# Performance work log

Hardware: AMD Instinct MI355X
Metric: run time of the kernel (lower is better)

The kernel has to match this reference:

```python
import jax, jax.numpy as jnp
import numpy as np

K_UPPER = 196608  # number of smallest-|grad| positions to mask per sample


def setup_inputs() -> dict:
    key = jax.random.key(0)
    k1, k2 = jax.random.split(key)
    x = jax.random.normal(k1, (64, 3, 512, 512), dtype=jnp.float32)
    grad = jax.random.normal(k2, (64, 3, 512, 512), dtype=jnp.float32)
    return {"x": x, "grad": grad}


def _mask_low_gradient(x, grad):
    # x, grad: [B, C, H, W]
    B, C, H, W = x.shape
    hw = H * W
    flat_g = grad.reshape(B, -1)                                  # [B, C*H*W]
    # _sort: k smallest absolute gradients -> top_k of negated abs (unsorted ok)
    _neg_vals, idx = jax.lax.top_k(-jnp.abs(flat_g), K_UPPER)     # idx: [B, K]
    # channel containing each selected flat index (matches the torch range test)
    ch = idx // hw                                                # [B, K]
    xc = x.reshape(B, C, hw)
    # Faithful to source: torch slice [start:channel_indexes] EXCLUDES the last
    # element of each channel when computing min/max.
    mn = jnp.min(xc[:, :, : hw - 1], axis=-1)                     # [B, C]
    mx = jnp.max(xc[:, :, : hw - 1], axis=-1)                     # [B, C]
    lo = jnp.take_along_axis(mn, ch, axis=1)                      # [B, K]
    hi = jnp.take_along_axis(mx, ch, axis=1)                      # [B, K]
    # uniform fill in [lo, hi) per masked element
    u = jax.random.uniform(jax.random.key(42), idx.shape, dtype=x.dtype)
    fill = lo + u * (hi - lo)                                     # [B, K]
    flat_x = x.reshape(B, -1)
    out = flat_x.at[jnp.arange(B)[:, None], idx].set(fill)
    return out.reshape(x.shape)


def reference(x, grad):
    return _mask_low_gradient(x, grad)
```

## Files before the change

kernel.cpp:

```cpp
#include <hip/hip_runtime.h>
#include <stdint.h>

#define TPB 256
#define TPS 1024

constexpr int BN   = 64;
constexpr int CCH  = 3;
constexpr int HWS  = 262144;
constexpr int LOG_HW = 18;
constexpr int NPS  = 786432;
constexpr int KSEL = 196608;
constexpr int KCAP = 200704;
constexpr int NB_T = 32;
constexpr int CH_T = NPS / NB_T;
constexpr int NB_C = 64;
constexpr int CH_C = NPS / NB_C;
constexpr int WCH  = CH_C / 4;
constexpr int NB_S = 8;
constexpr int CH_S = KCAP / NB_S;
constexpr int TILE = 4096;
constexpr int NBINS = 2048;
constexpr int SUB  = 8;

typedef unsigned u32x4 __attribute__((ext_vector_type(4)));

constexpr int WS_MN   = 0;
constexpr int WS_MX   = 192;
constexpr int WS_V1   = 384;
constexpr int WS_B1   = 448;
constexpr int WS_GS   = 512;
constexpr int WS_KP   = 576;
constexpr int WS_S0   = 640;
constexpr int WS_S01  = 704;
constexpr int WS_CNT  = 768;
constexpr int WS_COFF = WS_CNT + BN * 256;
constexpr int WS_MNP  = WS_COFF + BN * 256;
constexpr int WS_MXP  = WS_MNP + BN * CCH * SUB;
constexpr int WS_CHC  = WS_MXP + BN * CCH * SUB;
constexpr int WS_THA  = WS_CHC + BN * 4;
constexpr int WS_THB  = WS_THA + BN * NBINS;
constexpr int WS_H0   = WS_THB + BN * NBINS;
constexpr int WS_H1   = WS_H0 + BN * 256 * NB_S;
constexpr int WS_H2   = WS_H1 + BN * 256 * NB_S;
constexpr int WS_H3   = WS_H2 + BN * 256 * NB_S;
constexpr size_t WS_FIX_END = (size_t)WS_H3 + (size_t)BN * 256 * NB_S;
constexpr size_t RECW = (size_t)BN * KCAP * 2;
constexpr size_t WS_NEEDED_BYTES = (WS_FIX_END + 2 * RECW) * 4;

__device__ __forceinline__ unsigned rotl32(unsigned x, int r) { return (x << r) | (x >> (32 - r)); }

__device__ __forceinline__ void tf4(unsigned& x0, unsigned& x1, int a, int b, int c, int d) {
  x0 += x1; x1 = rotl32(x1, a); x1 ^= x0;
  x0 += x1; x1 = rotl32(x1, b); x1 ^= x0;
  x0 += x1; x1 = rotl32(x1, c); x1 ^= x0;
  x0 += x1; x1 = rotl32(x1, d); x1 ^= x0;
}

__device__ __forceinline__ void threefry2x32(unsigned k0, unsigned k1, unsigned c0, unsigned c1,
                                             unsigned& o0, unsigned& o1) {
  const unsigned ks2 = k0 ^ k1 ^ 0x1BD11BDAu;
  unsigned x0 = c0 + k0, x1 = c1 + k1;
  tf4(x0, x1, 13, 15, 26, 6);  x0 += k1;  x1 += ks2 + 1u;
  tf4(x0, x1, 17, 29, 16, 24); x0 += ks2; x1 += k0 + 2u;
  tf4(x0, x1, 13, 15, 26, 6);  x0 += k0;  x1 += k1 + 3u;
  tf4(x0, x1, 17, 29, 16, 24); x0 += k1;  x1 += ks2 + 4u;
  tf4(x0, x1, 13, 15, 26, 6);  x0 += ks2; x1 += k0 + 5u;
  o0 = x0; o1 = x1;
}

__global__ __launch_bounds__(TPB) void k_zero(unsigned* __restrict__ p, int n) {
  int i = blockIdx.x * TPB + threadIdx.x;
  if (i < n) p[i] = 0u;
}

__global__ __launch_bounds__(TPB) void k_mnmx(const float4* __restrict__ x,
                                              unsigned* __restrict__ ws) {
  __shared__ float smn[TPB], smx[TPB];
  const int g = blockIdx.x;
  const int bc = g / SUB, sub = g - bc * SUB;
  const int Q4 = HWS / 4 / SUB;
  const size_t base4 = (size_t)bc * (HWS / 4) + (size_t)sub * Q4;
  const bool last = (sub == SUB - 1);
  const int tid = threadIdx.x;
  float lo = 3.4e38f, hi = -3.4e38f;
  for (int i = tid; i < Q4; i += TPB) {
    float4 v = x[base4 + i];
    if (last && i == Q4 - 1) {
      lo = fminf(lo, fminf(fminf(v.x, v.y), v.z));
      hi = fmaxf(hi, fmaxf(fmaxf(v.x, v.y), v.z));
    } else {
      lo = fminf(lo, fminf(fminf(v.x, v.y), fminf(v.z, v.w)));
      hi = fmaxf(hi, fmaxf(fmaxf(v.x, v.y), fmaxf(v.z, v.w)));
    }
  }
  smn[tid] = lo; smx[tid] = hi; __syncthreads();
  for (int s = TPB / 2; s > 0; s >>= 1) {
    if (tid < s) { smn[tid] = fminf(smn[tid], smn[tid + s]); smx[tid] = fmaxf(smx[tid], smx[tid + s]); }
    __syncthreads();
  }
  if (tid == 0) {
    ((float*)(ws + WS_MNP))[g] = smn[0];
    ((float*)(ws + WS_MXP))[g] = smx[0];
  }
}

__global__ __launch_bounds__(TPB) void k_mnfin(unsigned* __restrict__ ws) {
  const int t = threadIdx.x;
  if (t < BN * CCH) {
    const float* mnp = (const float*)(ws + WS_MNP);
    const float* mxp = (const float*)(ws + WS_MXP);
    float lo = 3.4e38f, hi = -3.4e38f;
    for (int s = 0; s < SUB; ++s) {
      lo = fminf(lo, mnp[t * SUB + s]);
      hi = fmaxf(hi, mxp[t * SUB + s]);
    }
    ((float*)(ws + WS_MN))[t] = lo;
    ((float*)(ws + WS_MX))[t] = hi;
  }
}

__global__ __launch_bounds__(TPB) void k_thrA(const unsigned* __restrict__ gb, unsigned* __restrict__ hist) {
  __shared__ unsigned h[NBINS];
  const int b = blockIdx.y, blk = blockIdx.x, tid = threadIdx.x;
  for (int v = tid; v < NBINS; v += TPB) h[v] = 0u;
  __syncthreads();
  const uint4* g4 = (const uint4*)(gb + (size_t)b * NPS + (size_t)blk * CH_T);
  for (int i = tid; i < CH_T / 4; i += TPB) {
    uint4 v = g4[i];
    atomicAdd(&h[(v.x & 0x7FFFFFFFu) >> 21], 1u);
    atomicAdd(&h[(v.y & 0x7FFFFFFFu) >> 21], 1u);
    atomicAdd(&h[(v.z & 0x7FFFFFFFu) >> 21], 1u);
    atomicAdd(&h[(v.w & 0x7FFFFFFFu) >> 21], 1u);
  }
  __syncthreads();
  unsigned* gh = hist + (size_t)b * NBINS;
  for (int v = tid; v < NBINS; v += TPB) if (h[v]) atomicAdd(&gh[v], h[v]);
}

__global__ __launch_bounds__(TPB) void k_thrB(const unsigned* __restrict__ gb,
                                              unsigned* __restrict__ hist,
                                              const unsigned* __restrict__ ws) {
  __shared__ unsigned h[NBINS];
  const int b = blockIdx.y, blk = blockIdx.x, tid = threadIdx.x;
  for (int v = tid; v < NBINS; v += TPB) h[v] = 0u;
  __syncthreads();
  const unsigned sel = ws[WS_V1 + b];
  const uint4* g4 = (const uint4*)(gb + (size_t)b * NPS + (size_t)blk * CH_T);
  for (int i = tid; i < CH_T / 4; i += TPB) {
    uint4 v = g4[i];
    unsigned a0 = v.x & 0x7FFFFFFFu, a1 = v.y & 0x7FFFFFFFu;
    unsigned a2 = v.z & 0x7FFFFFFFu, a3 = v.w & 0x7FFFFFFFu;
    if ((a0 >> 21) == sel) atomicAdd(&h[(a0 >> 10) & 2047u], 1u);
    if ((a1 >> 21) == sel) atomicAdd(&h[(a1 >> 10) & 2047u], 1u);
    if ((a2 >> 21) == sel) atomicAdd(&h[(a2 >> 10) & 2047u], 1u);
    if ((a3 >> 21) == sel) atomicAdd(&h[(a3 >> 10) & 2047u], 1u);
  }
  __syncthreads();
  unsigned* gh = hist + (size_t)b * NBINS;
  for (int v = tid; v < NBINS; v += TPB) if (h[v]) atomicAdd(&gh[v], h[v]);
}

__global__ __launch_bounds__(TPB) void k_find(const unsigned* __restrict__ hist,
                                              unsigned* __restrict__ ws, int mode) {
  __shared__ unsigned part[TPB];
  const int b = blockIdx.x, tid = threadIdx.x;
  const unsigned* h = hist + (size_t)b * NBINS;
  const int per = NBINS / TPB;
  const unsigned Kt = (mode == 0) ? (unsigned)KSEL : (unsigned)KSEL - ws[WS_B1 + b];
  unsigned vals[8];
  unsigned s = 0;
  for (int j = 0; j < per; ++j) { vals[j] = h[tid * per + j]; s += vals[j]; }
  part[tid] = s; __syncthreads();
  for (int off = 1; off < TPB; off <<= 1) {
    unsigned t = (tid >= off) ? part[tid - off] : 0u;
    __syncthreads(); part[tid] += t; __syncthreads();
  }
  unsigned run = part[tid] - s;
  for (int j = 0; j < per; ++j) {
    const unsigned lo = run, c = vals[j];
    run += c;
    if (lo < Kt && Kt <= run) {
      const unsigned v = (unsigned)(tid * per + j);
      if (mode == 0) {
        ws[WS_V1 + b] = v; ws[WS_B1 + b] = lo;
      } else {
        const unsigned T22 = (ws[WS_V1 + b] << 11) | v;
        ws[WS_GS + b] = (T22 << 10) | 1023u;
        unsigned kp = ws[WS_B1 + b] + lo + c;
        if (kp > (unsigned)KCAP) kp = (unsigned)KCAP;
        ws[WS_KP + b] = kp;
      }
    }
  }
}

__global__ __launch_bounds__(TPB) void k_ccount(const unsigned* __restrict__ gb, unsigned* __restrict__ ws) {
  __shared__ unsigned chs[3];
  const int bid = blockIdx.x;
  const int b = bid & 63, blk = bid >> 6, tid = threadIdx.x;
  const int lane = tid & 63, wv = tid >> 6;
  if (tid < 3) chs[tid] = 0u;
  __syncthreads();
  const unsigned G = ws[WS_GS + b];
  const uint4* g4 = (const uint4*)(gb + (size_t)b * NPS + (size_t)blk * CH_C) + wv * (WCH / 4);
  const unsigned e0 = (unsigned)blk * CH_C + (unsigned)wv * WCH;
  unsigned cnt = 0, cc0 = 0, cc1 = 0, cc2 = 0;
  for (int it = 0; it < WCH / 256; ++it) {
    const uint4 v = g4[it * 64 + lane];
    const unsigned e = e0 + (unsigned)it * 256u + (unsigned)lane * 4u;
    const unsigned k[4] = { v.x & 0x7FFFFFFFu, v.y & 0x7FFFFFFFu, v.z & 0x7FFFFFFFu, v.w & 0x7FFFFFFFu };
#pragma unroll
    for (int c = 0; c < 4; ++c) {
      if (k[c] <= G) {
        ++cnt;
        const unsigned ch = (e + (unsigned)c) >> LOG_HW;
        if (ch == 0) ++cc0; else if (ch == 1) ++cc1; else ++cc2;
      }
    }
  }
  for (int off = 32; off >= 1; off >>= 1) cnt += __shfl_down(cnt, off, 64);
  if (lane == 0) ws[WS_CNT + b * 256 + blk * 4 + wv] = cnt;
  if (cc0) atomicAdd(&chs[0], cc0);
  if (cc1) atomicAdd(&chs[1], cc1);
  if (cc2) atomicAdd(&chs[2], cc2);
  __syncthreads();
  if (tid < 3 && chs[tid]) atomicAdd(&ws[WS_CHC + b * 4 + tid], chs[tid]);
}

__global__ __launch_bounds__(TPB) void k_cscan(unsigned* __restrict__ ws) {
  __shared__ unsigned wsum[4];
  const int b = blockIdx.x, tid = threadIdx.x;
  const int lane = tid & 63, wv = tid >> 6;
  const unsigned cnt = ws[WS_CNT + b * 256 + tid];
  unsigned incl = cnt;
  for (int off = 1; off < 64; off <<= 1) {
    unsigned t = __shfl_up(incl, off, 64);
    if (lane >= off) incl += t;
  }
  if (lane == 63) wsum[wv] = incl;
  __syncthreads();
  unsigned wpre = 0;
  for (int w = 0; w < wv; ++w) wpre += wsum[w];
  ws[WS_COFF + b * 256 + tid] = incl - cnt + wpre;
  if (tid == 0) {
    const unsigned s0 = ws[WS_CHC + b * 4 + 0];
    ws[WS_S0 + b] = s0;
    ws[WS_S01 + b] = s0 + ws[WS_CHC + b * 4 + 1];
  }
}

__global__ __launch_bounds__(TPB) void k_cscatter(const unsigned* __restrict__ gb,
                                                  const unsigned* __restrict__ ws,
                                                  unsigned* __restrict__ keyArr,
                                                  unsigned* __restrict__ H0) {
  __shared__ unsigned h2[256 * NB_S];
  const int bid = blockIdx.x;
  const int b = bid & 63, blk = bid >> 6, tid = threadIdx.x;
  const int lane = tid & 63, wv = tid >> 6;
  for (int e = tid; e < 256 * NB_S; e += TPB) h2[e] = 0u;
  __syncthreads();
  const unsigned G = ws[WS_GS + b];
  unsigned base = ws[WS_COFF + b * 256 + blk * 4 + wv];
  const uint4* g4 = (const uint4*)(gb + (size_t)b * NPS + (size_t)blk * CH_C) + wv * (WCH / 4);
  unsigned* ka = keyArr + (size_t)b * KCAP;
  for (int it = 0; it < WCH / 256; ++it) {
    const uint4 v = g4[it * 64 + lane];
    unsigned k[4] = { v.x & 0x7FFFFFFFu, v.y & 0x7FFFFFFFu, v.z & 0x7FFFFFFFu, v.w & 0x7FFFFFFFu };
    bool s[4];
    unsigned cnt = 0;
#pragma unroll
    for (int c = 0; c < 4; ++c) { s[c] = (k[c] <= G); cnt += (unsigned)s[c]; }
    unsigned incl = cnt;
    for (int off = 1; off < 64; off <<= 1) {
      unsigned u = __shfl_up(incl, off, 64);
      if (lane >= off) incl += u;
    }
    const unsigned wtot = __shfl(incl, 63, 64);
    unsigned pos = base + incl - cnt;
#pragma unroll
    for (int c = 0; c < 4; ++c) {
      if (s[c]) {
        if (pos < (unsigned)KCAP) {
          ka[pos] = k[c];
          atomicAdd(&h2[(k[c] & 255u) * NB_S + pos / (unsigned)CH_S], 1u);
        }
        ++pos;
      }
    }
    base += wtot;
  }
  __syncthreads();
  unsigned* Hb = H0 + (size_t)b * 256 * NB_S;
  for (int e = tid; e < 256 * NB_S; e += TPB) {
    unsigned c = h2[e];
    if (c) atomicAdd(&Hb[e], c);
  }
}

__global__ __launch_bounds__(TPB) void k_hscan(unsigned* __restrict__ H) {
  __shared__ unsigned wsum[4];
  const int b = blockIdx.x, tid = threadIdx.x;
  const int lane = tid & 63, wv = tid >> 6;
  unsigned* Hb = H + (size_t)b * 256 * NB_S;
  unsigned row[NB_S];
  unsigned run = 0;
#pragma unroll
  for (int k = 0; k < NB_S; ++k) {
    unsigned t = Hb[tid * NB_S + k];
    row[k] = run; run += t;
  }
  unsigned incl = run;
  for (int off = 1; off < 64; off <<= 1) {
    unsigned t = __shfl_up(incl, off, 64);
    if (lane >= off) incl += t;
  }
  if (lane == 63) wsum[wv] = incl;
  __syncthreads();
  unsigned wpre = 0;
  for (int w = 0; w < wv; ++w) wpre += wsum[w];
  const unsigned excl = incl - run + wpre;
#pragma unroll
  for (int k = 0; k < NB_S; ++k) Hb[tid * NB_S + k] = row[k] + excl;
}

template<int MODE>
__global__ __launch_bounds__(TPS) void k_sort8(const unsigned* __restrict__ keyIn,
                                               const uint2* __restrict__ inR,
                                               uint2* __restrict__ outR,
                                               unsigned* __restrict__ fillmap,
                                               const unsigned* __restrict__ Hcur,
                                               unsigned* __restrict__ Hnext,
                                               const unsigned* __restrict__ ws,
                                               int shift) {
  constexpr int DBITS = (MODE == 2) ? 7 : 8;
  constexpr unsigned DMASK = (1u << DBITS) - 1u;
  __shared__ unsigned wh[16][256];
  __shared__ unsigned gout[256];
  __shared__ unsigned gbase[256];
  __shared__ unsigned wsum[4];
  __shared__ uint2    stg[(MODE == 2) ? 1 : TILE];
  __shared__ unsigned h2[(MODE == 2) ? 1 : 256 * NB_S];
  const int bid = blockIdx.x;
  const int b = bid & 63, blk = bid >> 6, tid = threadIdx.x;
  const int lane = tid & 63, wv = tid >> 6;
  const unsigned long long ltm = (1ull << lane) - 1ull;
  const unsigned kp = min(ws[WS_KP + b], (unsigned)KCAP);
  const unsigned s0 = (unsigned)blk * CH_S;
  const unsigned s1 = min(s0 + (unsigned)CH_S, kp);
  const unsigned* ki = keyIn + (size_t)b * KCAP;
  const uint2* in = inR + (size_t)b * KCAP;
  uint2* out = outR + (size_t)b * KCAP;
  unsigned* fm = fillmap + (size_t)b * KCAP;

  unsigned S0 = 0, S01 = 0;
  float l0 = 0, l1 = 0, l2 = 0, h0 = 0, h1 = 0, h2v = 0;
  if (MODE == 2) {
    S0 = ws[WS_S0 + b]; S01 = ws[WS_S01 + b];
    const float* mnf = (const float*)(ws + WS_MN);
    const float* mxf = (const float*)(ws + WS_MX);
    l0 = mnf[b * CCH]; l1 = mnf[b * CCH + 1]; l2 = mnf[b * CCH + 2];
    h0 = mxf[b * CCH]; h1 = mxf[b * CCH + 1]; h2v = mxf[b * CCH + 2];
  }

  for (int d = tid; d < 256; d += TPS) gbase[d] = Hcur[((size_t)b * 256 + d) * NB_S + blk];
  if (MODE != 2) for (int e = tid; e < 256 * NB_S; e += TPS) h2[e] = 0u;
  __syncthreads();

  for (unsigned t0 = s0; t0 < s1; t0 += (unsigned)TILE) {
    { uint4* w4 = (uint4*)&wh[0][0];
      w4[tid] = make_uint4(0u, 0u, 0u, 0u); }
    __syncthreads();

    unsigned key[4], cpp[4], wloc[4], dig[4];
    bool val[4];
    const unsigned wbase = t0 + (unsigned)wv * 256u;
#pragma unroll
    for (int c = 0; c < 4; ++c) {
      const unsigned i = wbase + (unsigned)c * 64u + (unsigned)lane;
      val[c] = (i < s1);
      if (MODE == 0) { cpp[c] = i; key[c] = val[c] ? ki[i] : 0u; }
      else { uint2 r = val[c] ? in[i] : make_uint2(0u, 0u); cpp[c] = r.x; key[c] = r.y; }
      dig[c] = (key[c] >> shift) & DMASK;
      unsigned long long peers = __ballot(val[c]);
#pragma unroll
      for (int bit = 0; bit < DBITS; ++bit) {
        unsigned long long bb = __ballot(val[c] && ((dig[c] >> bit) & 1u));
        peers &= ((dig[c] >> bit) & 1u) ? bb : ~bb;
      }
      const unsigned before = (unsigned)__popcll(peers & ltm);
      int ldr = __ffsll((unsigned long long)peers) - 1;
      if (ldr < 0) ldr = 0;
      unsigned old = 0;
      if (val[c] && lane == ldr) old = atomicAdd(&wh[wv][dig[c]], (unsigned)__popcll(peers));
      old = __shfl(old, ldr, 64);
      wloc[c] = old + before;
    }
    __syncthreads();

    unsigned incl = 0, tot = 0;
    if (tid < 256) {
      const unsigned d = (unsigned)tid;
#pragma unroll
      for (int w = 0; w < 16; ++w) tot += wh[w][d];
      incl = tot;
      for (int off = 1; off < 64; off <<= 1) {
        unsigned t = __shfl_up(incl, off, 64);
        if (lane >= off) incl += t;
      }
      if (lane == 63) wsum[wv] = incl;
    }
    __syncthreads();
    if (tid < 256) {
      const unsigned d = (unsigned)tid;
      unsigned wpre = 0;
      for (int w = 0; w < wv; ++w) wpre += wsum[w];
      const unsigned tstart = incl - tot + wpre;
      const unsigned g = gbase[d];
      gout[d] = g - tstart;
      gbase[d] = g + tot;
      unsigned run = tstart;
#pragma unroll
      for (int w = 0; w < 16; ++w) { const unsigned t = wh[w][d]; wh[w][d] = run; run += t; }
    }
    __syncthreads();

    if (MODE != 2) {
#pragma unroll
      for (int c = 0; c < 4; ++c) {
        if (val[c]) {
          uint2 r; r.x = cpp[c]; r.y = key[c];
          stg[wh[wv][dig[c]] + wloc[c]] = r;
        }
      }
      __syncthreads();
      const unsigned nt = min((unsigned)TILE, s1 - t0);
      for (unsigned j = tid; j < nt; j += TPS) {
        const uint2 r = stg[j];
        const unsigned d = (r.y >> shift) & 255u;
        const unsigned pos = gout[d] + j;
        out[pos] = r;
        const unsigned nd = (r.y >> (shift + 8)) & 255u;
        atomicAdd(&h2[nd * NB_S + pos / (unsigned)CH_S], 1u);
      }
    } else {
#pragma unroll
      for (int c = 0; c < 4; ++c) {
        if (val[c]) {
          const unsigned rank = gout[dig[c]] + wh[wv][dig[c]] + wloc[c];
          unsigned res = 0xFFFFFFFFu;
          if (rank < (unsigned)KSEL) {
            const unsigned p = (unsigned)b * (unsigned)KSEL + rank;
            unsigned o0, o1;
            threefry2x32(0u, 42u, 0u, p, o0, o1);
            const unsigned bits = o0 ^ o1;
            const float u = __uint_as_float((bits >> 9) | 0x3f800000u) - 1.0f;
            const unsigned ch = (unsigned)(cpp[c] >= S0) + (unsigned)(cpp[c] >= S01);
            const float lo = (ch == 0) ? l0 : ((ch == 1) ? l1 : l2);
            const float hi = (ch == 0) ? h0 : ((ch == 1) ? h1 : h2v);
            res = __float_as_uint(lo + u * (hi - lo));
          }
          fm[cpp[c]] = res;
        }
      }
    }
    __syncthreads();
  }

  if (MODE != 2) {
    unsigned* Hb = Hnext + (size_t)b * 256 * NB_S;
    for (int e = tid; e < 256 * NB_S; e += TPS) {
      unsigned c = h2[e];
      if (c) atomicAdd(&Hb[e], c);
    }
  }
}

__global__ __launch_bounds__(TPB) void k_fill(const u32x4* __restrict__ x4,
                                              const u32x4* __restrict__ g4all,
                                              const unsigned* __restrict__ fillmap,
                                              const unsigned* __restrict__ ws,
                                              u32x4* __restrict__ out4) {
  const int bid = blockIdx.x;
  const int b = bid & 63, blk = bid >> 6, tid = threadIdx.x;
  const int lane = tid & 63, wv = tid >> 6;
  const unsigned G = ws[WS_GS + b];
  const unsigned kp = min(ws[WS_KP + b], (unsigned)KCAP);
  unsigned base = ws[WS_COFF + b * 256 + blk * 4 + wv];
  const size_t t4 = (size_t)b * (NPS / 4) + (size_t)blk * (CH_C / 4) + (size_t)wv * (WCH / 4);
  const unsigned* fm = fillmap + (size_t)b * KCAP;
  for (int it = 0; it < WCH / 256; ++it) {
    const size_t a = t4 + it * 64 + lane;
    const u32x4 gv = __builtin_nontemporal_load(&g4all[a]);
    u32x4 xv = __builtin_nontemporal_load(&x4[a]);
    unsigned k[4] = { gv.x & 0x7FFFFFFFu, gv.y & 0x7FFFFFFFu, gv.z & 0x7FFFFFFFu, gv.w & 0x7FFFFFFFu };
    bool s[4];
    unsigned cnt = 0;
#pragma unroll
    for (int c = 0; c < 4; ++c) { s[c] = (k[c] <= G); cnt += (unsigned)s[c]; }
    unsigned incl = cnt;
    for (int off = 1; off < 64; off <<= 1) {
      unsigned u = __shfl_up(incl, off, 64);
      if (lane >= off) incl += u;
    }
    const unsigned wtot = __shfl(incl, 63, 64);
    unsigned pos = base + incl - cnt;
#pragma unroll
    for (int c = 0; c < 4; ++c) {
      if (s[c]) {
        if (pos < kp) {
          const unsigned r = fm[pos];
          if (r != 0xFFFFFFFFu) xv[c] = r;
        }
        ++pos;
      }
    }
    __builtin_nontemporal_store(xv, &out4[a]);
    base += wtot;
  }
}

extern "C" void kernel_launch(void* const* d_in, const int* in_sizes, int n_in,
                              void* d_out, int out_size, void* d_ws, size_t ws_size,
                              hipStream_t stream) {
  const float* x = (const float*)d_in[0];
  const unsigned* gb = (const unsigned*)d_in[1];
  float* out = (float*)d_out;
  unsigned* ws = (unsigned*)d_ws;
  if (ws_size < WS_NEEDED_BYTES) return;

  unsigned* R1 = ws + WS_FIX_END;
  unsigned* R2 = ws + WS_FIX_END + RECW;
  unsigned* H0 = ws + WS_H0;
  unsigned* H1 = ws + WS_H1;
  unsigned* H2 = ws + WS_H2;
  unsigned* H3 = ws + WS_H3;

  dim3 blk(TPB);
  dim3 sblk(TPS);

  k_mnmx<<<dim3(BN * CCH * SUB), blk, 0, stream>>>((const float4*)x, ws);
  k_mnfin<<<dim3(1), blk, 0, stream>>>(ws);
  {
    const int nz = (int)(WS_FIX_END - WS_CHC);
    k_zero<<<dim3((nz + TPB - 1) / TPB), blk, 0, stream>>>(ws + WS_CHC, nz);
  }

  k_thrA<<<dim3(NB_T, BN), blk, 0, stream>>>(gb, ws + WS_THA);
  k_find<<<dim3(BN), blk, 0, stream>>>(ws + WS_THA, ws, 0);
  k_thrB<<<dim3(NB_T, BN), blk, 0, stream>>>(gb, ws + WS_THB, ws);
  k_find<<<dim3(BN), blk, 0, stream>>>(ws + WS_THB, ws, 1);

  k_ccount<<<dim3(NB_C * BN), blk, 0, stream>>>(gb, ws);
  k_cscan<<<dim3(BN), blk, 0, stream>>>(ws);
  k_cscatter<<<dim3(NB_C * BN), blk, 0, stream>>>(gb, ws, R1, H0);

  k_hscan<<<dim3(BN), blk, 0, stream>>>(H0);
  k_sort8<0><<<dim3(NB_S * BN), sblk, 0, stream>>>(R1, (const uint2*)nullptr, (uint2*)R2, nullptr, H0, H1, ws, 0);
  k_hscan<<<dim3(BN), blk, 0, stream>>>(H1);
  k_sort8<1><<<dim3(NB_S * BN), sblk, 0, stream>>>(nullptr, (const uint2*)R2, (uint2*)R1, nullptr, H1, H2, ws, 8);
  k_hscan<<<dim3(BN), blk, 0, stream>>>(H2);
  k_sort8<1><<<dim3(NB_S * BN), sblk, 0, stream>>>(nullptr, (const uint2*)R1, (uint2*)R2, nullptr, H2, H3, ws, 16);
  k_hscan<<<dim3(BN), blk, 0, stream>>>(H3);
  k_sort8<2><<<dim3(NB_S * BN), sblk, 0, stream>>>(nullptr, (const uint2*)R2, (uint2*)nullptr, R1, H3, nullptr, ws, 24);

  k_fill<<<dim3(NB_C * BN), blk, 0, stream>>>((const u32x4*)x, (const u32x4*)gb, R1, ws, (u32x4*)out);
}
```

Measured before the change: 768.6 us.

## Replace scattered fillmap writes with bucketed pair scatter and local unpack

The final radix pass used to write fill values straight into the fillmap at random candidate positions. It now runs a dedicated k_final kernel that computes the rank-based fill values and then buckets (position, value) pairs by position block of 4096, using histograms gathered during the third sort pass. A new k_unpack kernel then scatters each bucket through shared memory and writes the fillmap with coalesced stores. The aim is to turn uncoalesced global scatter writes into coalesced ones, at the cost of an extra kernel, an extra scan, extra histogram atomics and a round trip through the pair buffer.

New measurement: 774.0 us. Within noise of the previous version (+0.7%).

```diff
diff --git a/kernel.cpp b/kernel.cpp
--- a/kernel.cpp
+++ b/kernel.cpp
@@ -21,6 +21,7 @@
 constexpr int TILE = 4096;
 constexpr int NBINS = 2048;
 constexpr int SUB  = 8;
+constexpr int NFB  = 49;
 
 typedef unsigned u32x4 __attribute__((ext_vector_type(4)));
 
@@ -43,7 +44,8 @@
 constexpr int WS_H1   = WS_H0 + BN * 256 * NB_S;
 constexpr int WS_H2   = WS_H1 + BN * 256 * NB_S;
 constexpr int WS_H3   = WS_H2 + BN * 256 * NB_S;
-constexpr size_t WS_FIX_END = (size_t)WS_H3 + (size_t)BN * 256 * NB_S;
+constexpr int WS_HF   = WS_H3 + BN * 256 * NB_S;
+constexpr size_t WS_FIX_END = (size_t)WS_HF + (size_t)BN * 64 * NB_S;
 constexpr size_t RECW = (size_t)BN * KCAP * 2;
 constexpr size_t WS_NEEDED_BYTES = (WS_FIX_END + 2 * RECW) * 4;
 
@@ -323,23 +325,46 @@
   for (int k = 0; k < NB_S; ++k) Hb[tid * NB_S + k] = row[k] + excl;
 }
 
+__global__ __launch_bounds__(64) void k_hscanF(unsigned* __restrict__ Hf) {
+  const int b = blockIdx.x, tid = threadIdx.x;
+  unsigned* Hb = Hf + (size_t)b * 64 * NB_S;
+  unsigned row[NB_S];
+  unsigned run = 0;
+  if (tid < NFB) {
+#pragma unroll
+    for (int k = 0; k < NB_S; ++k) {
+      unsigned t = Hb[tid * NB_S + k];
+      row[k] = run; run += t;
+    }
+  }
+  unsigned incl = run;
+  for (int off = 1; off < 64; off <<= 1) {
+    unsigned t = __shfl_up(incl, off, 64);
+    if (tid >= off) incl += t;
+  }
+  const unsigned excl = incl - run;
+  if (tid < NFB) {
+#pragma unroll
+    for (int k = 0; k < NB_S; ++k) Hb[tid * NB_S + k] = row[k] + excl;
+  }
+}
+
 template<int MODE>
 __global__ __launch_bounds__(TPS) void k_sort8(const unsigned* __restrict__ keyIn,
                                                const uint2* __restrict__ inR,
                                                uint2* __restrict__ outR,
-                                               unsigned* __restrict__ fillmap,
                                                const unsigned* __restrict__ Hcur,
                                                unsigned* __restrict__ Hnext,
+                                               unsigned* __restrict__ Hf,
                                                const unsigned* __restrict__ ws,
                                                int shift) {
-  constexpr int DBITS = (MODE == 2) ? 7 : 8;
-  constexpr unsigned DMASK = (1u << DBITS) - 1u;
   __shared__ unsigned wh[16][256];
   __shared__ unsigned gout[256];
   __shared__ unsigned gbase[256];
   __shared__ unsigned wsum[4];
-  __shared__ uint2    stg[(MODE == 2) ? 1 : TILE];
-  __shared__ unsigned h2[(MODE == 2) ? 1 : 256 * NB_S];
+  __shared__ uint2    stg[TILE];
+  __shared__ unsigned h2[256 * NB_S];
+  __shared__ unsigned h2f[(MODE == 1) ? NFB * NB_S : 1];
   const int bid = blockIdx.x;
   const int b = bid & 63, blk = bid >> 6, tid = threadIdx.x;
   const int lane = tid & 63, wv = tid >> 6;
@@ -350,20 +375,11 @@
   const unsigned* ki = keyIn + (size_t)b * KCAP;
   const uint2* in = inR + (size_t)b * KCAP;
   uint2* out = outR + (size_t)b * KCAP;
-  unsigned* fm = fillmap + (size_t)b * KCAP;
-
-  unsigned S0 = 0, S01 = 0;
-  float l0 = 0, l1 = 0, l2 = 0, h0 = 0, h1 = 0, h2v = 0;
-  if (MODE == 2) {
-    S0 = ws[WS_S0 + b]; S01 = ws[WS_S01 + b];
-    const float* mnf = (const float*)(ws + WS_MN);
-    const float* mxf = (const float*)(ws + WS_MX);
-    l0 = mnf[b * CCH]; l1 = mnf[b * CCH + 1]; l2 = mnf[b * CCH + 2];
-    h0 = mxf[b * CCH]; h1 = mxf[b * CCH + 1]; h2v = mxf[b * CCH + 2];
-  }
+  const bool doF = (MODE == 1) && (Hf != nullptr);
 
   for (int d = tid; d < 256; d += TPS) gbase[d] = Hcur[((size_t)b * 256 + d) * NB_S + blk];
-  if (MODE != 2) for (int e = tid; e < 256 * NB_S; e += TPS) h2[e] = 0u;
+  for (int e = tid; e < 256 * NB_S; e += TPS) h2[e] = 0u;
+  if (MODE == 1) { if (doF) for (int e = tid; e < NFB * NB_S; e += TPS) h2f[e] = 0u; }
   __syncthreads();
 
   for (unsigned t0 = s0; t0 < s1; t0 += (unsigned)TILE) {
@@ -380,10 +396,10 @@
       val[c] = (i < s1);
       if (MODE == 0) { cpp[c] = i; key[c] = val[c] ? ki[i] : 0u; }
       else { uint2 r = val[c] ? in[i] : make_uint2(0u, 0u); cpp[c] = r.x; key[c] = r.y; }
-      dig[c] = (key[c] >> shift) & DMASK;
+      dig[c] = (key[c] >> shift) & 255u;
       unsigned long long peers = __ballot(val[c]);
 #pragma unroll
-      for (int bit = 0; bit < DBITS; ++bit) {
+      for (int bit = 0; bit < 8; ++bit) {
         unsigned long long bb = __ballot(val[c] && ((dig[c] >> bit) & 1u));
         peers &= ((dig[c] >> bit) & 1u) ? bb : ~bb;
       }
@@ -424,55 +440,210 @@
     }
     __syncthreads();
 
-    if (MODE != 2) {
-#pragma unroll
-      for (int c = 0; c < 4; ++c) {
-        if (val[c]) {
-          uint2 r; r.x = cpp[c]; r.y = key[c];
-          stg[wh[wv][dig[c]] + wloc[c]] = r;
-        }
-      }
-      __syncthreads();
-      const unsigned nt = min((unsigned)TILE, s1 - t0);
-      for (unsigned j = tid; j < nt; j += TPS) {
-        const uint2 r = stg[j];
-        const unsigned d = (r.y >> shift) & 255u;
-        const unsigned pos = gout[d] + j;
-        out[pos] = r;
-        const unsigned nd = (r.y >> (shift + 8)) & 255u;
-        atomicAdd(&h2[nd * NB_S + pos / (unsigned)CH_S], 1u);
-      }
-    } else {
-#pragma unroll
-      for (int c = 0; c < 4; ++c) {
-        if (val[c]) {
-          const unsigned rank = gout[dig[c]] + wh[wv][dig[c]] + wloc[c];
-          unsigned res = 0xFFFFFFFFu;
-          if (rank < (unsigned)KSEL) {
-            const unsigned p = (unsigned)b * (unsigned)KSEL + rank;
-            unsigned o0, o1;
-            threefry2x32(0u, 42u, 0u, p, o0, o1);
-            const unsigned bits = o0 ^ o1;
-            const float u = __uint_as_float((bits >> 9) | 0x3f800000u) - 1.0f;
-            const unsigned ch = (unsigned)(cpp[c] >= S0) + (unsigned)(cpp[c] >= S01);
-            const float lo = (ch == 0) ? l0 : ((ch == 1) ? l1 : l2);
-            const float hi = (ch == 0) ? h0 : ((ch == 1) ? h1 : h2v);
-            res = __float_as_uint(lo + u * (hi - lo));
-          }
-          fm[cpp[c]] = res;
-        }
-      }
-    }
-    __syncthreads();
-  }
-
-  if (MODE != 2) {
+#pragma unroll
+    for (int c = 0; c < 4; ++c) {
+      if (val[c]) {
+        uint2 r; r.x = cpp[c]; r.y = key[c];
+        stg[wh[wv][dig[c]] + wloc[c]] = r;
+      }
+    }
+    __syncthreads();
+    const unsigned nt = min((unsigned)TILE, s1 - t0);
+    for (unsigned j = tid; j < nt; j += TPS) {
+      const uint2 r = stg[j];
+      const unsigned d = (r.y >> shift) & 255u;
+      const unsigned pos = gout[d] + j;
+      out[pos] = r;
+      const unsigned nd = (r.y >> (shift + 8)) & 255u;
+      atomicAdd(&h2[nd * NB_S + pos / (unsigned)CH_S], 1u);
+      if (doF) atomicAdd(&h2f[(r.x >> 12) * NB_S + pos / (unsigned)CH_S], 1u);
+    }
+    __syncthreads();
+  }
+
+  {
     unsigned* Hb = Hnext + (size_t)b * 256 * NB_S;
     for (int e = tid; e < 256 * NB_S; e += TPS) {
       unsigned c = h2[e];
       if (c) atomicAdd(&Hb[e], c);
     }
-  }
+    if (doF) {
+      unsigned* Hfb = Hf + (size_t)b * 64 * NB_S;
+      for (int e = tid; e < NFB * NB_S; e += TPS) {
+        unsigned c = h2f[e];
+        if (c) atomicAdd(&Hfb[e], c);
+      }
+    }
+  }
+}
+
+__global__ __launch_bounds__(TPS) void k_final(const uint2* __restrict__ inR,
+                                               uint2* __restrict__ pairOut,
+                                               const unsigned* __restrict__ Hcur,
+                                               const unsigned* __restrict__ Hf,
+                                               const unsigned* __restrict__ ws) {
+  __shared__ unsigned wh[16][128];
+  __shared__ unsigned gbase[128];
+  __shared__ unsigned whF[16][64];
+  __shared__ unsigned goutF[64];
+  __shared__ unsigned gbaseF[64];
+  __shared__ uint2    stg[TILE];
+  const int bid = blockIdx.x;
+  const int b = bid & 63, blk = bid >> 6, tid = threadIdx.x;
+  const int lane = tid & 63, wv = tid >> 6;
+  const unsigned long long ltm = (1ull << lane) - 1ull;
+  const unsigned kp = min(ws[WS_KP + b], (unsigned)KCAP);
+  const unsigned s0 = (unsigned)blk * CH_S;
+  const unsigned s1 = min(s0 + (unsigned)CH_S, kp);
+  const uint2* in = inR + (size_t)b * KCAP;
+  uint2* po = pairOut + (size_t)b * KCAP;
+
+  const unsigned S0 = ws[WS_S0 + b], S01 = ws[WS_S01 + b];
+  const float* mnf = (const float*)(ws + WS_MN);
+  const float* mxf = (const float*)(ws + WS_MX);
+  const float l0 = mnf[b * CCH], l1 = mnf[b * CCH + 1], l2 = mnf[b * CCH + 2];
+  const float h0 = mxf[b * CCH], h1 = mxf[b * CCH + 1], h2v = mxf[b * CCH + 2];
+
+  for (int d = tid; d < 128; d += TPS) gbase[d] = Hcur[((size_t)b * 256 + d) * NB_S + blk];
+  for (int d = tid; d < 64; d += TPS)
+    gbaseF[d] = (d < NFB) ? Hf[((size_t)b * 64 + d) * NB_S + blk] : 0u;
+  __syncthreads();
+
+  for (unsigned t0 = s0; t0 < s1; t0 += (unsigned)TILE) {
+    { uint4* p = (uint4*)&wh[0][0];
+      if (tid < 512) p[tid] = make_uint4(0u, 0u, 0u, 0u);
+      uint4* q = (uint4*)&whF[0][0];
+      if (tid >= 512 && tid < 768) q[tid - 512] = make_uint4(0u, 0u, 0u, 0u); }
+    __syncthreads();
+
+    unsigned key[4], cpp[4], wloc[4], dig[4];
+    bool val[4];
+    const unsigned wbase = t0 + (unsigned)wv * 256u;
+#pragma unroll
+    for (int c = 0; c < 4; ++c) {
+      const unsigned i = wbase + (unsigned)c * 64u + (unsigned)lane;
+      val[c] = (i < s1);
+      uint2 r = val[c] ? in[i] : make_uint2(0u, 0u);
+      cpp[c] = r.x; key[c] = r.y;
+      dig[c] = (key[c] >> 24) & 127u;
+      unsigned long long peers = __ballot(val[c]);
+#pragma unroll
+      for (int bit = 0; bit < 7; ++bit) {
+        unsigned long long bb = __ballot(val[c] && ((dig[c] >> bit) & 1u));
+        peers &= ((dig[c] >> bit) & 1u) ? bb : ~bb;
+      }
+      const unsigned before = (unsigned)__popcll(peers & ltm);
+      int ldr = __ffsll((unsigned long long)peers) - 1;
+      if (ldr < 0) ldr = 0;
+      unsigned old = 0;
+      if (val[c] && lane == ldr) old = atomicAdd(&wh[wv][dig[c]], (unsigned)__popcll(peers));
+      old = __shfl(old, ldr, 64);
+      wloc[c] = old + before;
+    }
+    __syncthreads();
+
+    if (tid < 128) {
+      const unsigned d = (unsigned)tid;
+      unsigned run = gbase[d];
+#pragma unroll
+      for (int w = 0; w < 16; ++w) { const unsigned t = wh[w][d]; wh[w][d] = run; run += t; }
+      gbase[d] = run;
+    }
+    __syncthreads();
+
+    unsigned vfill[4], dbF[4], wlocF[4];
+#pragma unroll
+    for (int c = 0; c < 4; ++c) {
+      if (val[c]) {
+        const unsigned rank = wh[wv][dig[c]] + wloc[c];
+        unsigned res = 0xFFFFFFFFu;
+        if (rank < (unsigned)KSEL) {
+          const unsigned p = (unsigned)b * (unsigned)KSEL + rank;
+          unsigned o0, o1;
+          threefry2x32(0u, 42u, 0u, p, o0, o1);
+          const unsigned bits = o0 ^ o1;
+          const float u = __uint_as_float((bits >> 9) | 0x3f800000u) - 1.0f;
+          const unsigned ch = (unsigned)(cpp[c] >= S0) + (unsigned)(cpp[c] >= S01);
+          const float lo = (ch == 0) ? l0 : ((ch == 1) ? l1 : l2);
+          const float hi = (ch == 0) ? h0 : ((ch == 1) ? h1 : h2v);
+          res = __float_as_uint(lo + u * (hi - lo));
+        }
+        vfill[c] = res;
+      }
+      dbF[c] = cpp[c] >> 12;
+      unsigned long long peers = __ballot(val[c]);
+#pragma unroll
+      for (int bit = 0; bit < 6; ++bit) {
+        unsigned long long bb = __ballot(val[c] && ((dbF[c] >> bit) & 1u));
+        peers &= ((dbF[c] >> bit) & 1u) ? bb : ~bb;
+      }
+      const unsigned before = (unsigned)__popcll(peers & ltm);
+      int ldr = __ffsll((unsigned long long)peers) - 1;
+      if (ldr < 0) ldr = 0;
+      unsigned old = 0;
+      if (val[c] && lane == ldr) old = atomicAdd(&whF[wv][dbF[c]], (unsigned)__popcll(peers));
+      old = __shfl(old, ldr, 64);
+      wlocF[c] = old + before;
+    }
+    __syncthreads();
+
+    if (tid < 64) {
+      const unsigned d = (unsigned)tid;
+      unsigned tot = 0;
+      if (d < NFB) {
+#pragma unroll
+        for (int w = 0; w < 16; ++w) tot += whF[w][d];
+      }
+      unsigned incl = tot;
+      for (int off = 1; off < 64; off <<= 1) {
+        unsigned t = __shfl_up(incl, off, 64);
+        if (lane >= off) incl += t;
+      }
+      const unsigned tstart = incl - tot;
+      goutF[d] = gbaseF[d] - tstart;
+      gbaseF[d] += tot;
+      unsigned run = tstart;
+#pragma unroll
+      for (int w = 0; w < 16; ++w) { const unsigned t = whF[w][d]; whF[w][d] = run; run += t; }
+    }
+    __syncthreads();
+
+#pragma unroll
+    for (int c = 0; c < 4; ++c) {
+      if (val[c]) {
+        uint2 r; r.x = cpp[c]; r.y = vfill[c];
+        stg[whF[wv][dbF[c]] + wlocF[c]] = r;
+      }
+    }
+    __syncthreads();
+
+    const unsigned nt = min((unsigned)TILE, s1 - t0);
+    for (unsigned j = tid; j < nt; j += TPS) {
+      const uint2 r = stg[j];
+      po[goutF[r.x >> 12] + j] = r;
+    }
+    __syncthreads();
+  }
+}
+
+__global__ __launch_bounds__(TPB) void k_unpack(const uint2* __restrict__ pairs,
+                                                unsigned* __restrict__ fm,
+                                                const unsigned* __restrict__ ws) {
+  __shared__ unsigned vals[4096];
+  const int bid = blockIdx.x;
+  const int b = bid & 63, d = bid >> 6, tid = threadIdx.x;
+  const unsigned kp = min(ws[WS_KP + b], (unsigned)KCAP);
+  const unsigned start = (unsigned)d * 4096u;
+  if (start >= kp) return;
+  const unsigned cnt = min(4096u, kp - start);
+  const uint2* pb = pairs + (size_t)b * KCAP + start;
+  for (unsigned j = tid; j < cnt; j += TPB) {
+    const uint2 r = pb[j];
+    vals[r.x & 4095u] = r.y;
+  }
+  __syncthreads();
+  unsigned* f = fm + (size_t)b * KCAP + start;
+  for (unsigned j = tid; j < cnt; j += TPB) f[j] = vals[j];
 }
 
 __global__ __launch_bounds__(TPB) void k_fill(const u32x4* __restrict__ x4,
@@ -534,6 +705,7 @@
   unsigned* H1 = ws + WS_H1;
   unsigned* H2 = ws + WS_H2;
   unsigned* H3 = ws + WS_H3;
+  unsigned* HF = ws + WS_HF;
 
   dim3 blk(TPB);
   dim3 sblk(TPS);
@@ -555,13 +727,16 @@
   k_cscatter<<<dim3(NB_C * BN), blk, 0, stream>>>(gb, ws, R1, H0);
 
   k_hscan<<<dim3(BN), blk, 0, stream>>>(H0);
-  k_sort8<0><<<dim3(NB_S * BN), sblk, 0, stream>>>(R1, (const uint2*)nullptr, (uint2*)R2, nullptr, H0, H1, ws, 0);
+  k_sort8<0><<<dim3(NB_S * BN), sblk, 0, stream>>>(R1, (const uint2*)nullptr, (uint2*)R2, H0, H1, nullptr, ws, 0);
   k_hscan<<<dim3(BN), blk, 0, stream>>>(H1);
-  k_sort8<1><<<dim3(NB_S * BN), sblk, 0, stream>>>(nullptr, (const uint2*)R2, (uint2*)R1, nullptr, H1, H2, ws, 8);
+  k_sort8<1><<<dim3(NB_S * BN), sblk, 0, stream>>>(nullptr, (const uint2*)R2, (uint2*)R1, H1, H2, nullptr, ws, 8);
   k_hscan<<<dim3(BN), blk, 0, stream>>>(H2);
-  k_sort8<1><<<dim3(NB_S * BN), sblk, 0, stream>>>(nullptr, (const uint2*)R1, (uint2*)R2, nullptr, H2, H3, ws, 16);
+  k_sort8<1><<<dim3(NB_S * BN), sblk, 0, stream>>>(nullptr, (const uint2*)R1, (uint2*)R2, H2, H3, HF, ws, 16);
   k_hscan<<<dim3(BN), blk, 0, stream>>>(H3);
-  k_sort8<2><<<dim3(NB_S * BN), sblk, 0, stream>>>(nullptr, (const uint2*)R2, (uint2*)nullptr, R1, H3, nullptr, ws, 24);
-
-  k_fill<<<dim3(NB_C * BN), blk, 0, stream>>>((const u32x4*)x, (const u32x4*)gb, R1, ws, (u32x4*)out);
-}
+  k_hscanF<<<dim3(BN), dim3(64), 0, stream>>>(HF);
+
+  k_final<<<dim3(NB_S * BN), sblk, 0, stream>>>((const uint2*)R2, (uint2*)R1, H3, HF, ws);
+  k_unpack<<<dim3(NFB * BN), blk, 0, stream>>>((const uint2*)R1, R2, ws);
+
+  k_fill<<<dim3(NB_C * BN), blk, 0, stream>>>((const u32x4*)x, (const u32x4*)gb, R2, ws, (u32x4*)out);
+}
```
